# Kernel optimization log

Measured on AMD Instinct MI355X. Metric: run time of the kernel, lower is better.

## Reference

```python
import jax, jax.numpy as jnp
import numpy as np

D_K = 128  # query/key dim, used for the 1/sqrt(d_k) scale


def setup_inputs() -> dict:
    key = jax.random.key(0)
    k1, k2, k3, k4 = jax.random.split(key, 4)
    B, L, d_model, d_k, d_v = 4, 2048, 1024, 128, 128

    def xavier(k, shape):
        # matches nn.init.xavier_uniform_ for 2D weights
        limit = np.sqrt(6.0 / (shape[0] + shape[1]))
        return jax.random.uniform(k, shape, jnp.float32, -limit, limit)

    return {
        "X": jax.random.normal(k1, (B, L, d_model), jnp.float32),
        "W_Q": xavier(k2, (d_model, d_k)),
        "W_K": xavier(k3, (d_model, d_k)),
        "W_V": xavier(k4, (d_model, d_v)),
    }


def reference(X, W_Q, W_K, W_V):
    # X: (B, L, d_model)
    L = X.shape[1]
    Q = jnp.einsum("bld,dk->blk", X, W_Q)          # (B, L, d_k)
    K = jnp.einsum("bld,dk->blk", X, W_K)          # (B, L, d_k)
    V = jnp.einsum("bld,dv->blv", X, W_V)          # (B, L, d_v)
    scale = D_K ** -0.5
    scores = jnp.einsum("bqk,bpk->bqp", Q, K) * scale  # (B, L, L)
    # causal mask: positions above the diagonal set to -inf
    causal = jnp.tril(jnp.ones((L, L), dtype=bool))
    scores = jnp.where(causal, scores, -jnp.inf)
    A = jax.nn.softmax(scores, axis=-1)            # (B, L, L)
    Z = jnp.einsum("bqp,bpv->bqv", A, V)           # (B, L, d_v)
    return Z
```

## Files before the change

### kernel.cpp

```cpp
#include <hip/hip_runtime.h>
#include <hip/hip_bf16.h>

typedef __bf16 bf16;
typedef __attribute__((ext_vector_type(4))) __bf16 bf16x4;
typedef __attribute__((ext_vector_type(8))) __bf16 bf16x8;
typedef __attribute__((ext_vector_type(4))) float f32x4;

#define D_MODEL 1024
#define DK 128
#define LSEQ 2048
#define NQT 128
#define NB 4
#define SCALE2 (0.08838834764831845f * 1.4426950408889634f)

__global__ __launch_bounds__(256) void wt_kernel(
    const float* __restrict__ Wq, const float* __restrict__ Wk,
    const float* __restrict__ Wv, bf16* __restrict__ Wt)
{
    __shared__ bf16 tile[64][72];
    const float* W = (blockIdx.z == 0) ? Wq : (blockIdx.z == 1) ? Wk : Wv;
    int k0 = blockIdx.x * 64;
    int n0 = blockIdx.y * 64;
    int t  = threadIdx.x;
    #pragma unroll
    for (int i = 0; i < 16; ++i) {
        int idx = t + i * 256;
        int r = idx >> 6, c = idx & 63;
        tile[c][r] = (bf16)W[(size_t)(k0 + r) * DK + n0 + c];
    }
    __syncthreads();
    bf16* out = Wt + (size_t)blockIdx.z * DK * D_MODEL;
    #pragma unroll
    for (int i = 0; i < 16; ++i) {
        int idx = t + i * 256;
        int rr = idx >> 6, cc = idx & 63;
        out[(size_t)(n0 + rr) * D_MODEL + k0 + cc] = tile[rr][cc];
    }
}

__global__ __launch_bounds__(256) void proj_kernel(
    const float* __restrict__ X, const bf16* __restrict__ Wt,
    bf16* __restrict__ Qs, bf16* __restrict__ Kb, bf16* __restrict__ Vt)
{
    __shared__ bf16 Xs[64][72];
    __shared__ bf16 Ws[128][72];
    int mt = blockIdx.x, mat = blockIdx.y;
    const bf16* W = Wt + (size_t)mat * DK * D_MODEL;
    int t = threadIdx.x;
    int wave = t >> 6, lane = t & 63;
    int lq = lane & 15, g = lane >> 4;
    int row0 = mt * 64;

    f32x4 acc[4][2];
    #pragma unroll
    for (int m = 0; m < 4; ++m)
        #pragma unroll
        for (int n = 0; n < 2; ++n) acc[m][n] = f32x4{0.f, 0.f, 0.f, 0.f};

    f32x4  rxf[4];
    bf16x8 rw[4];
    auto LOADR = [&](int k0) {
        #pragma unroll
        for (int i = 0; i < 4; ++i) {
            int u = t + i * 256, r = u >> 4, c4 = u & 15;
            rxf[i] = *reinterpret_cast<const f32x4*>(
                &X[(size_t)(row0 + r) * D_MODEL + k0 + c4 * 4]);
        }
        #pragma unroll
        for (int i = 0; i < 4; ++i) {
            int u = t + i * 256, r = u >> 3, c8 = u & 7;
            rw[i] = *reinterpret_cast<const bf16x8*>(
                &W[(size_t)r * D_MODEL + k0 + c8 * 8]);
        }
    };
    auto STORER = [&]() {
        #pragma unroll
        for (int i = 0; i < 4; ++i) {
            int u = t + i * 256, r = u >> 4, c4 = u & 15;
            bf16x4 h;
            h[0]=(bf16)rxf[i][0]; h[1]=(bf16)rxf[i][1];
            h[2]=(bf16)rxf[i][2]; h[3]=(bf16)rxf[i][3];
            *reinterpret_cast<bf16x4*>(&Xs[r][c4 * 4]) = h;
        }
        #pragma unroll
        for (int i = 0; i < 4; ++i) {
            int u = t + i * 256, r = u >> 3, c8 = u & 7;
            *reinterpret_cast<bf16x8*>(&Ws[r][c8 * 8]) = rw[i];
        }
    };

    LOADR(0);
    for (int ks = 0; ks < 16; ++ks) {
        __syncthreads();
        STORER();
        if (ks + 1 < 16) LOADR((ks + 1) * 64);
        __syncthreads();
        #pragma unroll
        for (int kk = 0; kk < 2; ++kk) {
            bf16x8 a[4];
            #pragma unroll
            for (int mr = 0; mr < 4; ++mr)
                a[mr] = *reinterpret_cast<const bf16x8*>(&Xs[mr * 16 + lq][kk * 32 + g * 8]);
            #pragma unroll
            for (int n = 0; n < 2; ++n) {
                bf16x8 bfr = *reinterpret_cast<const bf16x8*>(
                    &Ws[wave * 32 + n * 16 + lq][kk * 32 + g * 8]);
                #pragma unroll
                for (int mr = 0; mr < 4; ++mr)
                    acc[mr][n] = __builtin_amdgcn_mfma_f32_16x16x32_bf16(a[mr], bfr, acc[mr][n], 0, 0, 0);
            }
        }
    }
    #pragma unroll
    for (int mr = 0; mr < 4; ++mr) {
        int orow = row0 + mr * 16 + g * 4;
        #pragma unroll
        for (int n = 0; n < 2; ++n) {
            int col = wave * 32 + n * 16 + lq;
            if (mat == 0) {
                #pragma unroll
                for (int r = 0; r < 4; ++r)
                    Qs[(size_t)(orow + r) * DK + col] = (bf16)(acc[mr][n][r] * SCALE2);
            } else if (mat == 1) {
                #pragma unroll
                for (int r = 0; r < 4; ++r)
                    Kb[(size_t)(orow + r) * DK + col] = (bf16)acc[mr][n][r];
            } else {
                int bb  = orow >> 11;
                int kv0 = orow & 2047;
                bf16x4 h;
                h[0]=(bf16)acc[mr][n][0]; h[1]=(bf16)acc[mr][n][1];
                h[2]=(bf16)acc[mr][n][2]; h[3]=(bf16)acc[mr][n][3];
                *reinterpret_cast<bf16x4*>(
                    &Vt[((size_t)bb * DK + col) * LSEQ + kv0]) = h;
            }
        }
    }
}

__global__ __launch_bounds__(256, 3) void attn_kernel(
    const bf16* __restrict__ Qs, const bf16* __restrict__ Kb,
    const bf16* __restrict__ Vt, float* __restrict__ Zp,
    float* __restrict__ Mp, float* __restrict__ Lp,
    float* __restrict__ Out, int split)
{
    __shared__ bf16 Ks[64][136];
    __shared__ bf16 Vs[128][72];
    __shared__ bf16 P[4][16][72];
    int bid = blockIdx.x;
    int b, qblk, s;
    if (split) {
        int xcd = bid & 7, u = bid >> 3;
        b = xcd >> 1;
        int n2 = (u << 1) | (xcd & 1);
        int q = 0, off = 0;
        while (off + ((q >> 2) + 1) <= n2) { off += (q >> 2) + 1; ++q; }
        qblk = q;
        s = n2 - off;
    } else {
        b = bid >> 5;
        qblk = bid & 31;
        s = 0;
    }
    int t = threadIdx.x;
    int wave = t >> 6, lane = t & 63;
    int lq = lane & 15, g = lane >> 4;
    int qw16 = qblk * 4 + wave;
    int qg = qw16 * 16 + lq;

    int nt = qblk + 1;
    int t0 = split ? 4 * s : 0;
    int t1 = split ? min(4 * s + 4, nt) : nt;

    const bf16* Kbase = Kb + (size_t)b * LSEQ * DK;
    const bf16* Vbase = Vt + (size_t)b * DK * LSEQ;

    const bf16* Qrow = Qs + ((size_t)b * LSEQ + qg) * DK;
    bf16x8 qf[4];
    #pragma unroll
    for (int ks = 0; ks < 4; ++ks)
        qf[ks] = *reinterpret_cast<const bf16x8*>(&Qrow[ks * 32 + g * 8]);

    f32x4 z[8];
    #pragma unroll
    for (int i = 0; i < 8; ++i) z[i] = f32x4{0.f, 0.f, 0.f, 0.f};
    float mrun = -3.0e38f, lrun = 0.f;

    bf16x8 kreg[4], vreg[4];
    auto LOADKV = [&](int kvb) {
        #pragma unroll
        for (int i = 0; i < 4; ++i) {
            int u = t + i * 256, r = u >> 4, c = u & 15;
            kreg[i] = *reinterpret_cast<const bf16x8*>(
                &Kbase[(size_t)(kvb + r) * DK + c * 8]);
        }
        #pragma unroll
        for (int i = 0; i < 4; ++i) {
            int u = t + i * 256, d = u >> 3, c = u & 7;
            vreg[i] = *reinterpret_cast<const bf16x8*>(
                &Vbase[(size_t)d * LSEQ + kvb + c * 8]);
        }
    };
    auto STOREKV = [&]() {
        #pragma unroll
        for (int i = 0; i < 4; ++i) {
            int u = t + i * 256, r = u >> 4, c = u & 15;
            *reinterpret_cast<bf16x8*>(&Ks[r][c * 8]) = kreg[i];
        }
        #pragma unroll
        for (int i = 0; i < 4; ++i) {
            int u = t + i * 256, d = u >> 3, c = u & 7;
            *reinterpret_cast<bf16x8*>(&Vs[d][c * 8]) = vreg[i];
        }
    };

    LOADKV(t0 * 64);
    for (int ti = t0; ti < t1; ++ti) {
        int kvb = ti * 64;
        __syncthreads();
        STOREKV();
        if (ti + 1 < t1) LOADKV((ti + 1) * 64);
        __syncthreads();

        f32x4 sc[4];
        #pragma unroll
        for (int jj = 0; jj < 4; ++jj) sc[jj] = f32x4{0.f, 0.f, 0.f, 0.f};
        __builtin_amdgcn_s_setprio(1);
        #pragma unroll
        for (int jj = 0; jj < 4; ++jj)
            #pragma unroll
            for (int ks = 0; ks < 4; ++ks) {
                bf16x8 a = *reinterpret_cast<const bf16x8*>(
                    &Ks[jj * 16 + lq][ks * 32 + g * 8]);
                sc[jj] = __builtin_amdgcn_mfma_f32_16x16x32_bf16(a, qf[ks], sc[jj], 0, 0, 0);
            }
        __builtin_amdgcn_s_setprio(0);

        float sv[16];
        if (ti == nt - 1) {
            #pragma unroll
            for (int jj = 0; jj < 4; ++jj)
                #pragma unroll
                for (int r = 0; r < 4; ++r) {
                    int kv0 = kvb + jj * 16 + g * 4 + r;
                    sv[jj * 4 + r] = (kv0 <= qg) ? sc[jj][r] : -3.0e38f;
                }
        } else {
            #pragma unroll
            for (int jj = 0; jj < 4; ++jj)
                #pragma unroll
                for (int r = 0; r < 4; ++r) sv[jj * 4 + r] = sc[jj][r];
        }
        float mt = sv[0];
        #pragma unroll
        for (int i = 1; i < 16; ++i) mt = fmaxf(mt, sv[i]);
        mt = fmaxf(mt, __shfl_xor(mt, 16));
        mt = fmaxf(mt, __shfl_xor(mt, 32));
        if (!__all(mt <= mrun)) {
            float mnew  = fmaxf(mrun, mt);
            float alpha = exp2f(mrun - mnew);
            lrun *= alpha;
            #pragma unroll
            for (int i = 0; i < 8; ++i) {
                z[i][0] *= alpha; z[i][1] *= alpha; z[i][2] *= alpha; z[i][3] *= alpha;
            }
            mrun = mnew;
        }
        float psum = 0.f;
        #pragma unroll
        for (int jj = 0; jj < 4; ++jj) {
            bf16x4 pb;
            #pragma unroll
            for (int r = 0; r < 4; ++r) {
                float e = exp2f(sv[jj * 4 + r] - mrun);
                psum += e;
                pb[r] = (bf16)e;
            }
            *reinterpret_cast<bf16x4*>(&P[wave][lq][jj * 16 + g * 4]) = pb;
        }
        psum += __shfl_xor(psum, 16);
        psum += __shfl_xor(psum, 32);
        lrun += psum;
        __builtin_amdgcn_s_setprio(1);
        #pragma unroll
        for (int sl = 0; sl < 2; ++sl) {
            bf16x8 pf = *reinterpret_cast<const bf16x8*>(&P[wave][lq][sl * 32 + g * 8]);
            #pragma unroll
            for (int dt = 0; dt < 8; ++dt) {
                bf16x8 av = *reinterpret_cast<const bf16x8*>(
                    &Vs[dt * 16 + lq][sl * 32 + g * 8]);
                z[dt] = __builtin_amdgcn_mfma_f32_16x16x32_bf16(av, pf, z[dt], 0, 0, 0);
            }
        }
        __builtin_amdgcn_s_setprio(0);
    }

    if (!split) {
        float inv = 1.f / lrun;
        float* orow = Out + ((size_t)b * LSEQ + qg) * DK;
        #pragma unroll
        for (int dt = 0; dt < 8; ++dt) {
            f32x4 v;
            v[0]=z[dt][0]*inv; v[1]=z[dt][1]*inv; v[2]=z[dt][2]*inv; v[3]=z[dt][3]*inv;
            *reinterpret_cast<f32x4*>(&orow[dt * 16 + g * 4]) = v;
        }
    } else {
        size_t T = ((size_t)(b * NQT + qw16) * 8 + s);
        float* zp = Zp + T * (16 * 128);
        #pragma unroll
        for (int dt = 0; dt < 8; ++dt)
            *reinterpret_cast<f32x4*>(&zp[lq * 128 + dt * 16 + g * 4]) = z[dt];
        if (g == 0) {
            Mp[T * 16 + lq] = mrun;
            Lp[T * 16 + lq] = lrun;
        }
    }
}

__global__ __launch_bounds__(256) void combine_kernel(
    const float* __restrict__ Zp, const float* __restrict__ Mp,
    const float* __restrict__ Lp, float* __restrict__ Out)
{
    int qt = blockIdx.x, b = blockIdx.y;
    int S  = (qt >> 4) + 1;
    int t  = threadIdx.x;
    int r  = t >> 4;
    int d0 = (t & 15) * 8;
    size_t Tbase = (size_t)(b * NQT + qt) * 8;

    float m = -3.0e38f;
    for (int s = 0; s < S; ++s)
        m = fmaxf(m, Mp[(Tbase + s) * 16 + r]);

    float L = 0.f;
    f32x4 a0 = {0.f,0.f,0.f,0.f}, a1 = {0.f,0.f,0.f,0.f};
    for (int s = 0; s < S; ++s) {
        float w = exp2f(Mp[(Tbase + s) * 16 + r] - m);
        L += w * Lp[(Tbase + s) * 16 + r];
        const float* zp = Zp + (Tbase + s) * (16 * 128) + r * 128 + d0;
        f32x4 v0 = *reinterpret_cast<const f32x4*>(&zp[0]);
        f32x4 v1 = *reinterpret_cast<const f32x4*>(&zp[4]);
        a0[0]+=w*v0[0]; a0[1]+=w*v0[1]; a0[2]+=w*v0[2]; a0[3]+=w*v0[3];
        a1[0]+=w*v1[0]; a1[1]+=w*v1[1]; a1[2]+=w*v1[2]; a1[3]+=w*v1[3];
    }
    float inv = 1.f / L;
    float* orow = Out + ((size_t)b * LSEQ + qt * 16 + r) * DK + d0;
    f32x4 o0, o1;
    o0[0]=a0[0]*inv; o0[1]=a0[1]*inv; o0[2]=a0[2]*inv; o0[3]=a0[3]*inv;
    o1[0]=a1[0]*inv; o1[1]=a1[1]*inv; o1[2]=a1[2]*inv; o1[3]=a1[3]*inv;
    *reinterpret_cast<f32x4*>(&orow[0]) = o0;
    *reinterpret_cast<f32x4*>(&orow[4]) = o1;
}

extern "C" void kernel_launch(void* const* d_in, const int* in_sizes, int n_in,
                              void* d_out, int out_size, void* d_ws, size_t ws_size,
                              hipStream_t stream)
{
    const float* X  = (const float*)d_in[0];
    const float* Wq = (const float*)d_in[1];
    const float* Wk = (const float*)d_in[2];
    const float* Wv = (const float*)d_in[3];
    float* Out = (float*)d_out;

    char* ws = (char*)d_ws;
    bf16* Wt = (bf16*)(ws);
    bf16* Qs = (bf16*)(ws + ((size_t)1 << 20));
    bf16* Kb = (bf16*)(ws + ((size_t)3 << 20));
    bf16* Vt = (bf16*)(ws + ((size_t)5 << 20));
    size_t base = (size_t)7 << 20;

    size_t zp_bytes = (size_t)NB * NQT * 8 * 16 * 128 * 4;
    size_t ml_bytes = (size_t)NB * NQT * 8 * 16 * 4;
    int split = (ws_size >= base + zp_bytes + 2 * ml_bytes) ? 1 : 0;

    float* Zp = (float*)(ws + base);
    float* Mp = (float*)(ws + base + zp_bytes);
    float* Lp = (float*)(ws + base + zp_bytes + ml_bytes);

    hipLaunchKernelGGL(wt_kernel,   dim3(16, 2, 3), dim3(256), 0, stream, Wq, Wk, Wv, Wt);
    hipLaunchKernelGGL(proj_kernel, dim3(128, 3),   dim3(256), 0, stream, X, Wt, Qs, Kb, Vt);
    hipLaunchKernelGGL(attn_kernel, dim3(split ? 576 : NB * 32), dim3(256), 0, stream,
                       Qs, Kb, Vt, Zp, Mp, Lp, Out, split);
    if (split)
        hipLaunchKernelGGL(combine_kernel, dim3(NQT, NB), dim3(256), 0, stream,
                           Zp, Mp, Lp, Out);
}
```

Measured before the change: 51.88 us.

## Double-buffer K in LDS, read V fragments from global, store partials in bf16

The attention loop now double-buffers K tiles in shared memory with one barrier per iteration instead of two. V fragments are loaded straight from global memory into registers, overlapping the softmax work, rather than staged through LDS. Split-KV partial outputs are written and read as bf16 instead of fp32, halving combine traffic. Risks include higher register pressure, uncoalesced global V reads, and lower partial-sum precision.

```diff
diff --git a/kernel.cpp b/kernel.cpp
--- a/kernel.cpp
+++ b/kernel.cpp
@@ -140,12 +140,11 @@
 
 __global__ __launch_bounds__(256, 3) void attn_kernel(
     const bf16* __restrict__ Qs, const bf16* __restrict__ Kb,
-    const bf16* __restrict__ Vt, float* __restrict__ Zp,
+    const bf16* __restrict__ Vt, bf16* __restrict__ Zp,
     float* __restrict__ Mp, float* __restrict__ Lp,
     float* __restrict__ Out, int split)
 {
-    __shared__ bf16 Ks[64][136];
-    __shared__ bf16 Vs[128][72];
+    __shared__ bf16 Ks[2][64][136];
     __shared__ bf16 P[4][16][72];
     int bid = blockIdx.x;
     int b, qblk, s;
@@ -186,41 +185,31 @@
     for (int i = 0; i < 8; ++i) z[i] = f32x4{0.f, 0.f, 0.f, 0.f};
     float mrun = -3.0e38f, lrun = 0.f;
 
-    bf16x8 kreg[4], vreg[4];
-    auto LOADKV = [&](int kvb) {
+    bf16x8 kreg[4];
+    auto LOADK = [&](int kvb) {
         #pragma unroll
         for (int i = 0; i < 4; ++i) {
             int u = t + i * 256, r = u >> 4, c = u & 15;
             kreg[i] = *reinterpret_cast<const bf16x8*>(
                 &Kbase[(size_t)(kvb + r) * DK + c * 8]);
         }
-        #pragma unroll
-        for (int i = 0; i < 4; ++i) {
-            int u = t + i * 256, d = u >> 3, c = u & 7;
-            vreg[i] = *reinterpret_cast<const bf16x8*>(
-                &Vbase[(size_t)d * LSEQ + kvb + c * 8]);
-        }
     };
-    auto STOREKV = [&]() {
+    auto STOREK = [&](int buf) {
         #pragma unroll
         for (int i = 0; i < 4; ++i) {
             int u = t + i * 256, r = u >> 4, c = u & 15;
-            *reinterpret_cast<bf16x8*>(&Ks[r][c * 8]) = kreg[i];
-        }
-        #pragma unroll
-        for (int i = 0; i < 4; ++i) {
-            int u = t + i * 256, d = u >> 3, c = u & 7;
-            *reinterpret_cast<bf16x8*>(&Vs[d][c * 8]) = vreg[i];
+            *reinterpret_cast<bf16x8*>(&Ks[buf][r][c * 8]) = kreg[i];
         }
     };
 
-    LOADKV(t0 * 64);
+    LOADK(t0 * 64);
+    STOREK(0);
+    __syncthreads();
+    if (t0 + 1 < t1) LOADK((t0 + 1) * 64);
+
+    int cur = 0;
     for (int ti = t0; ti < t1; ++ti) {
         int kvb = ti * 64;
-        __syncthreads();
-        STOREKV();
-        if (ti + 1 < t1) LOADKV((ti + 1) * 64);
-        __syncthreads();
 
         f32x4 sc[4];
         #pragma unroll
@@ -231,10 +220,16 @@
             #pragma unroll
             for (int ks = 0; ks < 4; ++ks) {
                 bf16x8 a = *reinterpret_cast<const bf16x8*>(
-                    &Ks[jj * 16 + lq][ks * 32 + g * 8]);
+                    &Ks[cur][jj * 16 + lq][ks * 32 + g * 8]);
                 sc[jj] = __builtin_amdgcn_mfma_f32_16x16x32_bf16(a, qf[ks], sc[jj], 0, 0, 0);
             }
         __builtin_amdgcn_s_setprio(0);
+
+        bf16x8 av0[8];
+        #pragma unroll
+        for (int dt = 0; dt < 8; ++dt)
+            av0[dt] = *reinterpret_cast<const bf16x8*>(
+                &Vbase[(size_t)(dt * 16 + lq) * LSEQ + kvb + g * 8]);
 
         float sv[16];
         if (ti == nt - 1) {
@@ -281,18 +276,30 @@
         psum += __shfl_xor(psum, 16);
         psum += __shfl_xor(psum, 32);
         lrun += psum;
+
+        if (ti + 1 < t1) STOREK(cur ^ 1);
+
         __builtin_amdgcn_s_setprio(1);
-        #pragma unroll
-        for (int sl = 0; sl < 2; ++sl) {
-            bf16x8 pf = *reinterpret_cast<const bf16x8*>(&P[wave][lq][sl * 32 + g * 8]);
-            #pragma unroll
-            for (int dt = 0; dt < 8; ++dt) {
-                bf16x8 av = *reinterpret_cast<const bf16x8*>(
-                    &Vs[dt * 16 + lq][sl * 32 + g * 8]);
-                z[dt] = __builtin_amdgcn_mfma_f32_16x16x32_bf16(av, pf, z[dt], 0, 0, 0);
-            }
-        }
+        bf16x8 pf0 = *reinterpret_cast<const bf16x8*>(&P[wave][lq][g * 8]);
+        #pragma unroll
+        for (int dt = 0; dt < 8; ++dt)
+            z[dt] = __builtin_amdgcn_mfma_f32_16x16x32_bf16(av0[dt], pf0, z[dt], 0, 0, 0);
+        bf16x8 av1[8];
+        #pragma unroll
+        for (int dt = 0; dt < 8; ++dt)
+            av1[dt] = *reinterpret_cast<const bf16x8*>(
+                &Vbase[(size_t)(dt * 16 + lq) * LSEQ + kvb + 32 + g * 8]);
+        bf16x8 pf1 = *reinterpret_cast<const bf16x8*>(&P[wave][lq][32 + g * 8]);
+        #pragma unroll
+        for (int dt = 0; dt < 8; ++dt)
+            z[dt] = __builtin_amdgcn_mfma_f32_16x16x32_bf16(av1[dt], pf1, z[dt], 0, 0, 0);
         __builtin_amdgcn_s_setprio(0);
+
+        if (ti + 1 < t1) {
+            __syncthreads();
+            if (ti + 2 < t1) LOADK((ti + 2) * 64);
+            cur ^= 1;
+        }
     }
 
     if (!split) {
@@ -306,10 +313,14 @@
         }
     } else {
         size_t T = ((size_t)(b * NQT + qw16) * 8 + s);
-        float* zp = Zp + T * (16 * 128);
-        #pragma unroll
-        for (int dt = 0; dt < 8; ++dt)
-            *reinterpret_cast<f32x4*>(&zp[lq * 128 + dt * 16 + g * 4]) = z[dt];
+        bf16* zp = Zp + T * (16 * 128);
+        #pragma unroll
+        for (int dt = 0; dt < 8; ++dt) {
+            bf16x4 h;
+            h[0]=(bf16)z[dt][0]; h[1]=(bf16)z[dt][1];
+            h[2]=(bf16)z[dt][2]; h[3]=(bf16)z[dt][3];
+            *reinterpret_cast<bf16x4*>(&zp[lq * 128 + dt * 16 + g * 4]) = h;
+        }
         if (g == 0) {
             Mp[T * 16 + lq] = mrun;
             Lp[T * 16 + lq] = lrun;
@@ -318,7 +329,7 @@
 }
 
 __global__ __launch_bounds__(256) void combine_kernel(
-    const float* __restrict__ Zp, const float* __restrict__ Mp,
+    const bf16* __restrict__ Zp, const float* __restrict__ Mp,
     const float* __restrict__ Lp, float* __restrict__ Out)
 {
     int qt = blockIdx.x, b = blockIdx.y;
@@ -333,21 +344,20 @@
         m = fmaxf(m, Mp[(Tbase + s) * 16 + r]);
 
     float L = 0.f;
-    f32x4 a0 = {0.f,0.f,0.f,0.f}, a1 = {0.f,0.f,0.f,0.f};
+    float a[8] = {0.f, 0.f, 0.f, 0.f, 0.f, 0.f, 0.f, 0.f};
     for (int s = 0; s < S; ++s) {
         float w = exp2f(Mp[(Tbase + s) * 16 + r] - m);
         L += w * Lp[(Tbase + s) * 16 + r];
-        const float* zp = Zp + (Tbase + s) * (16 * 128) + r * 128 + d0;
-        f32x4 v0 = *reinterpret_cast<const f32x4*>(&zp[0]);
-        f32x4 v1 = *reinterpret_cast<const f32x4*>(&zp[4]);
-        a0[0]+=w*v0[0]; a0[1]+=w*v0[1]; a0[2]+=w*v0[2]; a0[3]+=w*v0[3];
-        a1[0]+=w*v1[0]; a1[1]+=w*v1[1]; a1[2]+=w*v1[2]; a1[3]+=w*v1[3];
+        bf16x8 v = *reinterpret_cast<const bf16x8*>(
+            &Zp[(Tbase + s) * (16 * 128) + r * 128 + d0]);
+        #pragma unroll
+        for (int j = 0; j < 8; ++j) a[j] += w * (float)v[j];
     }
     float inv = 1.f / L;
     float* orow = Out + ((size_t)b * LSEQ + qt * 16 + r) * DK + d0;
     f32x4 o0, o1;
-    o0[0]=a0[0]*inv; o0[1]=a0[1]*inv; o0[2]=a0[2]*inv; o0[3]=a0[3]*inv;
-    o1[0]=a1[0]*inv; o1[1]=a1[1]*inv; o1[2]=a1[2]*inv; o1[3]=a1[3]*inv;
+    o0[0]=a[0]*inv; o0[1]=a[1]*inv; o0[2]=a[2]*inv; o0[3]=a[3]*inv;
+    o1[0]=a[4]*inv; o1[1]=a[5]*inv; o1[2]=a[6]*inv; o1[3]=a[7]*inv;
     *reinterpret_cast<f32x4*>(&orow[0]) = o0;
     *reinterpret_cast<f32x4*>(&orow[4]) = o1;
 }
@@ -369,11 +379,11 @@
     bf16* Vt = (bf16*)(ws + ((size_t)5 << 20));
     size_t base = (size_t)7 << 20;
 
-    size_t zp_bytes = (size_t)NB * NQT * 8 * 16 * 128 * 4;
+    size_t zp_bytes = (size_t)NB * NQT * 8 * 16 * 128 * 2;
     size_t ml_bytes = (size_t)NB * NQT * 8 * 16 * 4;
     int split = (ws_size >= base + zp_bytes + 2 * ml_bytes) ? 1 : 0;
 
-    float* Zp = (float*)(ws + base);
+    bf16*  Zp = (bf16*)(ws + base);
     float* Mp = (float*)(ws + base + zp_bytes);
     float* Lp = (float*)(ws + base + zp_bytes + ml_bytes);
 
```

Measured after the change: 63.57 us. +22.5%, slower.

## Fuse split-KV combine into attention kernel via last-block atomic counter

Applied to the files above, without the earlier changes.

Removes the separate combine kernel launch. Each split block writes its partial results, then increments a per-query-block atomic counter, and the last block to finish merges all partials and writes the output. Query blocks with a single split write the output directly and skip the partial buffers. In exchange it adds a memset launch for the counters, thread fences and an atomic, and the combine work is serialized onto whichever block finishes last.

```diff
diff --git a/kernel.cpp b/kernel.cpp
--- a/kernel.cpp
+++ b/kernel.cpp
@@ -142,11 +142,12 @@
     const bf16* __restrict__ Qs, const bf16* __restrict__ Kb,
     const bf16* __restrict__ Vt, float* __restrict__ Zp,
     float* __restrict__ Mp, float* __restrict__ Lp,
-    float* __restrict__ Out, int split)
+    unsigned int* __restrict__ Cnt, float* __restrict__ Out, int split)
 {
     __shared__ bf16 Ks[64][136];
     __shared__ bf16 Vs[128][72];
     __shared__ bf16 P[4][16][72];
+    __shared__ int lastFlag;
     int bid = blockIdx.x;
     int b, qblk, s;
     if (split) {
@@ -295,7 +296,8 @@
         __builtin_amdgcn_s_setprio(0);
     }
 
-    if (!split) {
+    int S = (qblk >> 2) + 1;
+    if (!split || S == 1) {
         float inv = 1.f / lrun;
         float* orow = Out + ((size_t)b * LSEQ + qg) * DK;
         #pragma unroll
@@ -304,52 +306,60 @@
             v[0]=z[dt][0]*inv; v[1]=z[dt][1]*inv; v[2]=z[dt][2]*inv; v[3]=z[dt][3]*inv;
             *reinterpret_cast<f32x4*>(&orow[dt * 16 + g * 4]) = v;
         }
-    } else {
-        size_t T = ((size_t)(b * NQT + qw16) * 8 + s);
-        float* zp = Zp + T * (16 * 128);
-        #pragma unroll
-        for (int dt = 0; dt < 8; ++dt)
-            *reinterpret_cast<f32x4*>(&zp[lq * 128 + dt * 16 + g * 4]) = z[dt];
-        if (g == 0) {
-            Mp[T * 16 + lq] = mrun;
-            Lp[T * 16 + lq] = lrun;
-        }
-    }
-}
-
-__global__ __launch_bounds__(256) void combine_kernel(
-    const float* __restrict__ Zp, const float* __restrict__ Mp,
-    const float* __restrict__ Lp, float* __restrict__ Out)
-{
-    int qt = blockIdx.x, b = blockIdx.y;
-    int S  = (qt >> 4) + 1;
-    int t  = threadIdx.x;
-    int r  = t >> 4;
-    int d0 = (t & 15) * 8;
-    size_t Tbase = (size_t)(b * NQT + qt) * 8;
+        return;
+    }
+
+    size_t T = ((size_t)(b * NQT + qw16) * 8 + s);
+    float* zp = Zp + T * (16 * 128);
+    #pragma unroll
+    for (int dt = 0; dt < 8; ++dt)
+        *reinterpret_cast<f32x4*>(&zp[lq * 128 + dt * 16 + g * 4]) = z[dt];
+    if (g == 0) {
+        Mp[T * 16 + lq] = mrun;
+        Lp[T * 16 + lq] = lrun;
+    }
+
+    __threadfence();
+    if (t == 0) {
+        unsigned int old = atomicAdd(&Cnt[b * 32 + qblk], 1u);
+        lastFlag = (old == (unsigned int)(S - 1));
+    }
+    __syncthreads();
+    if (!lastFlag) return;
+    __threadfence();
+
+    int r  = t >> 2;
+    int dg = t & 3;
+    int ri = r & 15;
+    size_t Tb = (size_t)(b * NQT + qblk * 4 + (r >> 4)) * 8;
 
     float m = -3.0e38f;
-    for (int s = 0; s < S; ++s)
-        m = fmaxf(m, Mp[(Tbase + s) * 16 + r]);
-
+    for (int ss = 0; ss < S; ++ss)
+        m = fmaxf(m, Mp[(Tb + ss) * 16 + ri]);
     float L = 0.f;
-    f32x4 a0 = {0.f,0.f,0.f,0.f}, a1 = {0.f,0.f,0.f,0.f};
-    for (int s = 0; s < S; ++s) {
-        float w = exp2f(Mp[(Tbase + s) * 16 + r] - m);
-        L += w * Lp[(Tbase + s) * 16 + r];
-        const float* zp = Zp + (Tbase + s) * (16 * 128) + r * 128 + d0;
-        f32x4 v0 = *reinterpret_cast<const f32x4*>(&zp[0]);
-        f32x4 v1 = *reinterpret_cast<const f32x4*>(&zp[4]);
-        a0[0]+=w*v0[0]; a0[1]+=w*v0[1]; a0[2]+=w*v0[2]; a0[3]+=w*v0[3];
-        a1[0]+=w*v1[0]; a1[1]+=w*v1[1]; a1[2]+=w*v1[2]; a1[3]+=w*v1[3];
+    f32x4 acc[8];
+    #pragma unroll
+    for (int j = 0; j < 8; ++j) acc[j] = f32x4{0.f, 0.f, 0.f, 0.f};
+    for (int ss = 0; ss < S; ++ss) {
+        float w = exp2f(Mp[(Tb + ss) * 16 + ri] - m);
+        L += w * Lp[(Tb + ss) * 16 + ri];
+        const float* zr = Zp + (Tb + ss) * (16 * 128) + ri * 128 + dg * 32;
+        #pragma unroll
+        for (int j = 0; j < 8; ++j) {
+            f32x4 v = *reinterpret_cast<const f32x4*>(&zr[j * 4]);
+            acc[j][0] += w * v[0]; acc[j][1] += w * v[1];
+            acc[j][2] += w * v[2]; acc[j][3] += w * v[3];
+        }
     }
     float inv = 1.f / L;
-    float* orow = Out + ((size_t)b * LSEQ + qt * 16 + r) * DK + d0;
-    f32x4 o0, o1;
-    o0[0]=a0[0]*inv; o0[1]=a0[1]*inv; o0[2]=a0[2]*inv; o0[3]=a0[3]*inv;
-    o1[0]=a1[0]*inv; o1[1]=a1[1]*inv; o1[2]=a1[2]*inv; o1[3]=a1[3]*inv;
-    *reinterpret_cast<f32x4*>(&orow[0]) = o0;
-    *reinterpret_cast<f32x4*>(&orow[4]) = o1;
+    float* orow = Out + ((size_t)b * LSEQ + qblk * 64 + r) * DK + dg * 32;
+    #pragma unroll
+    for (int j = 0; j < 8; ++j) {
+        f32x4 o;
+        o[0]=acc[j][0]*inv; o[1]=acc[j][1]*inv;
+        o[2]=acc[j][2]*inv; o[3]=acc[j][3]*inv;
+        *reinterpret_cast<f32x4*>(&orow[j * 4]) = o;
+    }
 }
 
 extern "C" void kernel_launch(void* const* d_in, const int* in_sizes, int n_in,
@@ -371,17 +381,17 @@
 
     size_t zp_bytes = (size_t)NB * NQT * 8 * 16 * 128 * 4;
     size_t ml_bytes = (size_t)NB * NQT * 8 * 16 * 4;
-    int split = (ws_size >= base + zp_bytes + 2 * ml_bytes) ? 1 : 0;
+    int split = (ws_size >= base + zp_bytes + 2 * ml_bytes + 512) ? 1 : 0;
 
     float* Zp = (float*)(ws + base);
     float* Mp = (float*)(ws + base + zp_bytes);
     float* Lp = (float*)(ws + base + zp_bytes + ml_bytes);
-
+    unsigned int* Cnt = (unsigned int*)(ws + base + zp_bytes + 2 * ml_bytes);
+
+    if (split)
+        hipMemsetAsync(Cnt, 0, NB * 32 * sizeof(unsigned int), stream);
     hipLaunchKernelGGL(wt_kernel,   dim3(16, 2, 3), dim3(256), 0, stream, Wq, Wk, Wv, Wt);
     hipLaunchKernelGGL(proj_kernel, dim3(128, 3),   dim3(256), 0, stream, X, Wt, Qs, Kb, Vt);
     hipLaunchKernelGGL(attn_kernel, dim3(split ? 576 : NB * 32), dim3(256), 0, stream,
-                       Qs, Kb, Vt, Zp, Mp, Lp, Out, split);
-    if (split)
-        hipLaunchKernelGGL(combine_kernel, dim3(NQT, NB), dim3(256), 0, stream,
-                           Zp, Mp, Lp, Out);
+                       Qs, Kb, Vt, Zp, Mp, Lp, Cnt, Out, split);
 }
```

Measured after the change: 139.8 us. 169% more time.
